# Optimization experiments

Measured on AMD Instinct MI355X. Metric: run time of the kernel, lower is better.

Reference implementation:

```python
import jax, jax.numpy as jnp
import numpy as np

N_NODES = 100000
N_EDGES = 1600000
D = 64
NUM_GROUPS = 2


def setup_inputs() -> dict:
    key = jax.random.key(0)
    k_h, k_ws, k_wg, k_src, k_dst, k_grp = jax.random.split(key, 6)
    h = jax.random.normal(k_h, (N_NODES, D), dtype=jnp.float32)
    # nn.Linear(in, out, bias=False) weights have shape [out, in]
    W_self = jax.random.normal(k_ws, (D, D), dtype=jnp.float32) * (1.0 / np.sqrt(D))
    W_groups = jax.random.normal(k_wg, (NUM_GROUPS, D, D), dtype=jnp.float32) * (1.0 / np.sqrt(D))
    src = jax.random.randint(k_src, (N_EDGES,), 0, N_NODES, dtype=jnp.int32)
    dst = jax.random.randint(k_dst, (N_EDGES,), 0, N_NODES, dtype=jnp.int32)
    group_labels = jax.random.randint(k_grp, (N_NODES,), 0, NUM_GROUPS, dtype=jnp.int32)
    return {"h": h, "W_self": W_self, "W_groups": W_groups,
            "src": src, "dst": dst, "group_labels": group_labels}


def reference(h, W_self, W_groups, src, dst, group_labels):
    # h: [N, d_in]; W_self: [d_out, d_in]; W_groups: [G, d_out, d_in]
    # Edge list (src, dst) replaces the DGL graph; message m_e = h[src_e],
    # transformed by W_groups[group[src_e]], scatter-added into dst_e.
    n_nodes = h.shape[0]
    num_groups = W_groups.shape[0]

    h_self = h @ W_self.T                       # [N, d_out]

    h_src = jnp.take(h, src, axis=0)            # [E, d_in] edge gather
    g_src = jnp.take(group_labels, src, axis=0)  # [E]

    h_agg = jnp.zeros((n_nodes, W_groups.shape[1]), dtype=h.dtype)
    for i in range(num_groups):  # small fixed loop over groups
        masked = jnp.where((g_src == i)[:, None], h_src, 0.0)  # [E, d_in]
        # Linearity lets us aggregate first, then transform (same math as
        # transforming each message then scatter_add, but far less compute).
        seg = jax.ops.segment_sum(masked, dst, num_segments=n_nodes)  # [N, d_in]
        h_agg = h_agg + seg @ W_groups[i].T      # [N, d_out]

    return h_self + h_agg
```

## Files before the change

### kernel.cpp

```cpp
#include <hip/hip_runtime.h>

#define N_NODES 100000
#define N_EDGES 1600000
#define D 64
#define NB 784
#define NR 8
#define CAPB_R 384
#define LCAP 64
#define LSTR 68
#define SRC_MASK 0x1FFFF
#define NBB 782
#define ZOFF (N_NODES * 32)

typedef unsigned int u32;
typedef short bfrag8 __attribute__((ext_vector_type(8)));
typedef float f32x4 __attribute__((ext_vector_type(4)));


__device__ inline u32 pk_bf16(float lo, float hi) {
    u32 a = __float_as_uint(lo);
    a = (a + 0x7fffu + ((a >> 16) & 1u)) >> 16;
    u32 b = __float_as_uint(hi);
    b = (b + 0x7fffu + ((b >> 16) & 1u)) & 0xffff0000u;
    return a | b;
}

__global__ __launch_bounds__(256) void prep(const float* __restrict__ h,
                                            const float* __restrict__ W_self,
                                            const float* __restrict__ W_groups,
                                            const int* __restrict__ src,
                                            const int* __restrict__ dst,
                                            const int* __restrict__ grp,
                                            int* __restrict__ bcnt,
                                            int* __restrict__ buckets,
                                            u32* __restrict__ h_bf,
                                            u32* __restrict__ Wc) {
    __shared__ int hist[NB];
    __shared__ int gbase[NB];
    const int tid = threadIdx.x;
    const int bx = blockIdx.x;

    if (bx < NBB) {
        const int r = bx & (NR - 1);
        for (int b = tid; b < NB; b += 256) hist[b] = 0;
        __syncthreads();

        int ent[8], bkt[8], rnk[8];
        const int e0 = bx * 2048;
#pragma unroll
        for (int i = 0; i < 8; ++i) {
            int e = e0 + tid + i * 256;
            if (e < N_EDGES) {
                int s = src[e], d = dst[e];
                int g = grp[s];
                bkt[i] = d >> 7;
                ent[i] = s | (g << 17) | ((d & 127) << 18);
                rnk[i] = atomicAdd(&hist[bkt[i]], 1);
            } else {
                bkt[i] = -1;
            }
        }
        __syncthreads();
        for (int b = tid; b < NB; b += 256) {
            int hc = hist[b];
            gbase[b] = hc ? atomicAdd(&bcnt[b * NR + r], hc) : 0;
        }
        __syncthreads();
#pragma unroll
        for (int i = 0; i < 8; ++i) {
            if (bkt[i] >= 0) {
                int pos = gbase[bkt[i]] + rnk[i];
                if (pos < CAPB_R)
                    buckets[(bkt[i] * NR + r) * CAPB_R + pos] = ent[i];
            }
        }
    } else if (bx < NBB + 12500) {
        int i = (bx - NBB) * 256 + tid;
        float2 v = reinterpret_cast<const float2*>(h)[i];
        h_bf[i] = pk_bf16(v.x, v.y);
    } else {
        for (int idx = tid; idx < 6144; idx += 256) {
            int j = idx / 96, kk = idx - j * 96;
            int k = kk * 2;
            float lo, hi;
            if (k < 64)       { lo = W_self[j * 64 + k];          hi = W_self[j * 64 + k + 1]; }
            else if (k < 128) { lo = W_groups[j * 64 + k - 64];   hi = W_groups[j * 64 + k - 63]; }
            else              { lo = W_groups[4096 + j * 64 + k - 128];
                                hi = W_groups[4096 + j * 64 + k - 127]; }
            Wc[j * 96 + kk] = pk_bf16(lo, hi);
        }
        if (tid < 32) h_bf[ZOFF + tid] = 0u;
    }
}

__global__ __launch_bounds__(256, 8) void gather_gemm(const u32* __restrict__ h_bf,
                                                      const int* __restrict__ bcnt,
                                                      const int* __restrict__ buckets,
                                                      const u32* __restrict__ Wc,
                                                      float* __restrict__ out) {
    __shared__ __align__(16) int lcsr[32 * LSTR];
    __shared__ int cnt0[32];
    __shared__ int cnt1[32];

    const int tid = threadIdx.x;
    const int cb = blockIdx.x >> 2;
    const int sub = blockIdx.x & 3;
    const int nbase = cb * 128 + sub * 32;
    if (nbase >= N_NODES) return;

    if (tid < 32) { cnt0[tid] = 0; cnt1[tid] = 0; }
    __syncthreads();

    {
        const int4 cA = *reinterpret_cast<const int4*>(bcnt + cb * NR);
        const int4 cB = *reinterpret_cast<const int4*>(bcnt + cb * NR + 4);
        int cns[NR] = { cA.x, cA.y, cA.z, cA.w, cB.x, cB.y, cB.z, cB.w };
#pragma unroll
        for (int r = 0; r < NR; ++r) {
            const int cnt = min(cns[r], CAPB_R);
            const int* bp = buckets + (cb * NR + r) * CAPB_R;
            for (int i = tid; i < cnt; i += 256) {
                int e = bp[i];
                if (((e >> 23) & 3) == sub) {
                    int nl = (e >> 18) & 31;
                    int off = (e & SRC_MASK) * 32;
                    if ((e >> 17) & 1) {
                        int s1 = atomicAdd(&cnt1[nl], 1);
                        if (s1 < LCAP) lcsr[nl * LSTR + (LCAP - 1 - s1)] = off;
                    } else {
                        int s0 = atomicAdd(&cnt0[nl], 1);
                        if (s0 < LCAP) lcsr[nl * LSTR + s0] = off;
                    }
                }
            }
        }
    }
    __syncthreads();

    const int wave = tid >> 6;
    const int lane = tid & 63;
    const int half = lane >> 5;
    const int c = lane & 31;

    for (int q = 0; q < 8; ++q) {
        const int nl = wave * 8 + q;
        const int base = nl * LSTR;
        const int c0 = min(cnt0[nl], LCAP);
        const int c1 = min(cnt1[nl], LCAP);
        const int imax = max(c0, c1);
        float a0l = 0.f, a0h = 0.f, a1l = 0.f, a1h = 0.f;

        for (int i = 0; i < imax; i += 8) {
            int offA[4], offB[4];
#pragma unroll
            for (int k = 0; k < 4; ++k) {
                int t = i + 2 * k + half;
                int vA = lcsr[base + t];
                int vB = lcsr[base + (LCAP - 1 - t)];
                offA[k] = (t < c0) ? vA : ZOFF;
                offB[k] = (t < c1) ? vB : ZOFF;
            }
            u32 xA[4], xB[4];
#pragma unroll
            for (int k = 0; k < 4; ++k) {
                xA[k] = h_bf[(size_t)(offA[k] + c)];
                xB[k] = h_bf[(size_t)(offB[k] + c)];
            }
#pragma unroll
            for (int k = 0; k < 4; ++k) {
                a0l += __uint_as_float(xA[k] << 16);
                a0h += __uint_as_float(xA[k] & 0xffff0000u);
                a1l += __uint_as_float(xB[k] << 16);
                a1h += __uint_as_float(xB[k] & 0xffff0000u);
            }
        }

        a0l += __shfl_xor(a0l, 32, 64);
        a0h += __shfl_xor(a0h, 32, 64);
        a1l += __shfl_xor(a1l, 32, 64);
        a1h += __shfl_xor(a1h, 32, 64);

        if (half == 0) {
            lcsr[base + c]      = (int)pk_bf16(a0l, a0h);
            lcsr[base + 32 + c] = (int)pk_bf16(a1l, a1h);
        }
    }
    __syncthreads();

    const int m = lane & 15;
    const int quad = lane >> 4;
    const int rowh = wave & 1;
    const int jth = wave >> 1;
    const int nl16 = rowh * 16 + m;
    const int arow = nbase + nl16;

    union Cvt { uint4 u; bfrag8 s; };
    bfrag8 a[6];
    const u32* ap = h_bf + (size_t)arow * 32 + quad * 4;
#pragma unroll
    for (int ks = 0; ks < 2; ++ks) {
        Cvt cv;
        cv.u = *reinterpret_cast<const uint4*>(ap + ks * 16);
        a[ks] = cv.s;
    }
#pragma unroll
    for (int ks = 2; ks < 6; ++ks) {
        Cvt cv;
        cv.u = *reinterpret_cast<const uint4*>(&lcsr[nl16 * LSTR + (ks - 2) * 16 + quad * 4]);
        a[ks] = cv.s;
    }

    f32x4 acc[2];
#pragma unroll
    for (int jj = 0; jj < 2; ++jj) acc[jj] = (f32x4){0.f, 0.f, 0.f, 0.f};

    const u32* wp = Wc + (size_t)m * 96 + quad * 4;
#pragma unroll
    for (int ks = 0; ks < 6; ++ks) {
#pragma unroll
        for (int jj = 0; jj < 2; ++jj) {
            Cvt cw;
            cw.u = *reinterpret_cast<const uint4*>(wp + (jth * 2 + jj) * 1536 + ks * 16);
            acc[jj] = __builtin_amdgcn_mfma_f32_16x16x32_bf16(a[ks], cw.s, acc[jj], 0, 0, 0);
        }
    }

    const int rbase = nbase + rowh * 16 + quad * 4;
#pragma unroll
    for (int jj = 0; jj < 2; ++jj) {
#pragma unroll
        for (int r = 0; r < 4; ++r) {
            out[(size_t)(rbase + r) * 64 + (jth * 2 + jj) * 16 + m] = acc[jj][r];
        }
    }
}

extern "C" void kernel_launch(void* const* d_in, const int* in_sizes, int n_in,
                              void* d_out, int out_size, void* d_ws, size_t ws_size,
                              hipStream_t stream) {
    const float* h        = (const float*)d_in[0];
    const float* W_self   = (const float*)d_in[1];
    const float* W_groups = (const float*)d_in[2];
    const int*   src      = (const int*)d_in[3];
    const int*   dst      = (const int*)d_in[4];
    const int*   grp      = (const int*)d_in[5];
    float*       out      = (float*)d_out;

    int* bcnt    = (int*)d_ws;
    int* buckets = bcnt + 8192;
    u32* h_bf    = (u32*)(buckets + NB * NR * CAPB_R);
    u32* Wc      = h_bf + (size_t)N_NODES * 32 + 32;

    hipMemsetAsync(bcnt, 0, NB * NR * sizeof(int), stream);

    prep<<<NBB + 12500 + 1, 256, 0, stream>>>(h, W_self, W_groups, src, dst, grp,
                                              bcnt, buckets, h_bf, Wc);
    gather_gemm<<<NB * 4, 256, 0, stream>>>(h_bf, bcnt, buckets, Wc, out);
}
```

Measured before the change: 180.8 us.

## Bucket edges per 32-node block and merge group loops into one pass

Edges are now bucketed directly by 32-node destination blocks (3125 buckets with 2 replicas) instead of 128-node buckets that four blocks each rescanned and filtered. This removes the redundant four-way bucket reads in gather_gemm. The gather loop now walks the two group lists back to back instead of padding both to the longer length, which avoids wasted zero-row loads. The costs are a larger shared histogram in prep and more contended atomics per replica. Per-replica capacity is unchanged, so overflow is unlikely.

```diff
diff --git a/kernel.cpp b/kernel.cpp
--- a/kernel.cpp
+++ b/kernel.cpp
@@ -3,8 +3,8 @@
 #define N_NODES 100000
 #define N_EDGES 1600000
 #define D 64
-#define NB 784
-#define NR 8
+#define NB2 3125
+#define NR 2
 #define CAPB_R 384
 #define LCAP 64
 #define LSTR 68
@@ -35,14 +35,14 @@
                                             int* __restrict__ buckets,
                                             u32* __restrict__ h_bf,
                                             u32* __restrict__ Wc) {
-    __shared__ int hist[NB];
-    __shared__ int gbase[NB];
+    __shared__ int hist[NB2];
+    __shared__ int gbase[NB2];
     const int tid = threadIdx.x;
     const int bx = blockIdx.x;
 
     if (bx < NBB) {
         const int r = bx & (NR - 1);
-        for (int b = tid; b < NB; b += 256) hist[b] = 0;
+        for (int b = tid; b < NB2; b += 256) hist[b] = 0;
         __syncthreads();
 
         int ent[8], bkt[8], rnk[8];
@@ -53,15 +53,15 @@
             if (e < N_EDGES) {
                 int s = src[e], d = dst[e];
                 int g = grp[s];
-                bkt[i] = d >> 7;
-                ent[i] = s | (g << 17) | ((d & 127) << 18);
+                bkt[i] = d >> 5;
+                ent[i] = s | (g << 17) | ((d & 31) << 18);
                 rnk[i] = atomicAdd(&hist[bkt[i]], 1);
             } else {
                 bkt[i] = -1;
             }
         }
         __syncthreads();
-        for (int b = tid; b < NB; b += 256) {
+        for (int b = tid; b < NB2; b += 256) {
             int hc = hist[b];
             gbase[b] = hc ? atomicAdd(&bcnt[b * NR + r], hc) : 0;
         }
@@ -99,39 +99,30 @@
                                                       const u32* __restrict__ Wc,
                                                       float* __restrict__ out) {
     __shared__ __align__(16) int lcsr[32 * LSTR];
-    __shared__ int cnt0[32];
-    __shared__ int cnt1[32];
+    __shared__ int cntg[64];
 
     const int tid = threadIdx.x;
-    const int cb = blockIdx.x >> 2;
-    const int sub = blockIdx.x & 3;
-    const int nbase = cb * 128 + sub * 32;
-    if (nbase >= N_NODES) return;
-
-    if (tid < 32) { cnt0[tid] = 0; cnt1[tid] = 0; }
+    const int cb = blockIdx.x;
+    const int nbase = cb * 32;
+
+    if (tid < 64) cntg[tid] = 0;
     __syncthreads();
 
     {
-        const int4 cA = *reinterpret_cast<const int4*>(bcnt + cb * NR);
-        const int4 cB = *reinterpret_cast<const int4*>(bcnt + cb * NR + 4);
-        int cns[NR] = { cA.x, cA.y, cA.z, cA.w, cB.x, cB.y, cB.z, cB.w };
+        const int2 cc = *reinterpret_cast<const int2*>(bcnt + cb * NR);
+        int cns[NR] = { cc.x, cc.y };
 #pragma unroll
         for (int r = 0; r < NR; ++r) {
             const int cnt = min(cns[r], CAPB_R);
             const int* bp = buckets + (cb * NR + r) * CAPB_R;
             for (int i = tid; i < cnt; i += 256) {
                 int e = bp[i];
-                if (((e >> 23) & 3) == sub) {
-                    int nl = (e >> 18) & 31;
-                    int off = (e & SRC_MASK) * 32;
-                    if ((e >> 17) & 1) {
-                        int s1 = atomicAdd(&cnt1[nl], 1);
-                        if (s1 < LCAP) lcsr[nl * LSTR + (LCAP - 1 - s1)] = off;
-                    } else {
-                        int s0 = atomicAdd(&cnt0[nl], 1);
-                        if (s0 < LCAP) lcsr[nl * LSTR + s0] = off;
-                    }
-                }
+                int nl = (e >> 18) & 31;
+                int g = (e >> 17) & 1;
+                int off = (e & SRC_MASK) * 32;
+                int idx = atomicAdd(&cntg[g * 32 + nl], 1);
+                int pos = g ? (LCAP - 1 - idx) : idx;
+                if (idx < LCAP) lcsr[nl * LSTR + pos] = off;
             }
         }
     }
@@ -145,33 +136,66 @@
     for (int q = 0; q < 8; ++q) {
         const int nl = wave * 8 + q;
         const int base = nl * LSTR;
-        const int c0 = min(cnt0[nl], LCAP);
-        const int c1 = min(cnt1[nl], LCAP);
-        const int imax = max(c0, c1);
+        const int c0 = min(cntg[nl], LCAP);
+        const int c1 = min(cntg[32 + nl], LCAP);
+        const int total = c0 + c1;
         float a0l = 0.f, a0h = 0.f, a1l = 0.f, a1h = 0.f;
 
-        for (int i = 0; i < imax; i += 8) {
-            int offA[4], offB[4];
-#pragma unroll
-            for (int k = 0; k < 4; ++k) {
-                int t = i + 2 * k + half;
-                int vA = lcsr[base + t];
-                int vB = lcsr[base + (LCAP - 1 - t)];
-                offA[k] = (t < c0) ? vA : ZOFF;
-                offB[k] = (t < c1) ? vB : ZOFF;
-            }
-            u32 xA[4], xB[4];
-#pragma unroll
-            for (int k = 0; k < 4; ++k) {
-                xA[k] = h_bf[(size_t)(offA[k] + c)];
-                xB[k] = h_bf[(size_t)(offB[k] + c)];
-            }
-#pragma unroll
-            for (int k = 0; k < 4; ++k) {
-                a0l += __uint_as_float(xA[k] << 16);
-                a0h += __uint_as_float(xA[k] & 0xffff0000u);
-                a1l += __uint_as_float(xB[k] << 16);
-                a1h += __uint_as_float(xB[k] & 0xffff0000u);
+        for (int i = 0; i < total; i += 8) {
+            if (i + 8 <= c0) {
+                int off[4];
+#pragma unroll
+                for (int k = 0; k < 4; ++k)
+                    off[k] = lcsr[base + i + 2 * k + half];
+                u32 x[4];
+#pragma unroll
+                for (int k = 0; k < 4; ++k) x[k] = h_bf[(size_t)(off[k] + c)];
+#pragma unroll
+                for (int k = 0; k < 4; ++k) {
+                    a0l += __uint_as_float(x[k] << 16);
+                    a0h += __uint_as_float(x[k] & 0xffff0000u);
+                }
+            } else if (i >= c0) {
+                int off[4];
+#pragma unroll
+                for (int k = 0; k < 4; ++k) {
+                    int u = i + 2 * k + half;
+                    int idx = (LCAP - 1 - (u - c0)) & (LCAP - 1);
+                    int v = lcsr[base + idx];
+                    off[k] = (u < total) ? v : ZOFF;
+                }
+                u32 x[4];
+#pragma unroll
+                for (int k = 0; k < 4; ++k) x[k] = h_bf[(size_t)(off[k] + c)];
+#pragma unroll
+                for (int k = 0; k < 4; ++k) {
+                    a1l += __uint_as_float(x[k] << 16);
+                    a1h += __uint_as_float(x[k] & 0xffff0000u);
+                }
+            } else {
+                int off[4];
+                bool fm[4];
+#pragma unroll
+                for (int k = 0; k < 4; ++k) {
+                    int u = i + 2 * k + half;
+                    bool f = u < c0;
+                    int idx = f ? u : ((LCAP - 1 - (u - c0)) & (LCAP - 1));
+                    int v = lcsr[base + idx];
+                    off[k] = (u < total) ? v : ZOFF;
+                    fm[k] = f;
+                }
+                u32 x[4];
+#pragma unroll
+                for (int k = 0; k < 4; ++k) x[k] = h_bf[(size_t)(off[k] + c)];
+#pragma unroll
+                for (int k = 0; k < 4; ++k) {
+                    float vl = __uint_as_float(x[k] << 16);
+                    float vh = __uint_as_float(x[k] & 0xffff0000u);
+                    a0l += fm[k] ? vl : 0.f;
+                    a0h += fm[k] ? vh : 0.f;
+                    a1l += fm[k] ? 0.f : vl;
+                    a1h += fm[k] ? 0.f : vh;
+                }
             }
         }
 
@@ -248,12 +272,12 @@
 
     int* bcnt    = (int*)d_ws;
     int* buckets = bcnt + 8192;
-    u32* h_bf    = (u32*)(buckets + NB * NR * CAPB_R);
+    u32* h_bf    = (u32*)(buckets + NB2 * NR * CAPB_R);
     u32* Wc      = h_bf + (size_t)N_NODES * 32 + 32;
 
-    hipMemsetAsync(bcnt, 0, NB * NR * sizeof(int), stream);
+    hipMemsetAsync(bcnt, 0, 8192 * sizeof(int), stream);
 
     prep<<<NBB + 12500 + 1, 256, 0, stream>>>(h, W_self, W_groups, src, dst, grp,
                                               bcnt, buckets, h_bf, Wc);
-    gather_gemm<<<NB * 4, 256, 0, stream>>>(h_bf, bcnt, buckets, Wc, out);
-}
+    gather_gemm<<<NB2, 256, 0, stream>>>(h_bf, bcnt, buckets, Wc, out);
+}
```

Result: slower. 192.3 us (+6.4%).

## Bucket edges per 32-node block and aggregate via LDS float atomics

Applied to the files above, without the earlier changes.

Edges are now binned directly into 32-node buckets with only two sub-ranks, and the two sub-counters are packed into one 32-bit word so a single atomic updates both. The gather kernel drops the per-block filter and local CSR build. Each wave instead reads bucket entries and scatter-adds bf16-expanded rows into an fp32 LDS segment buffer with shared atomics, then packs that buffer to bf16 for the MFMA stage. The h conversion uses float4 loads. This trades per-node sequential accumulation loops for many LDS atomic adds, and it raises the histogram size and the number of buckets.

```diff
diff --git a/kernel.cpp b/kernel.cpp
--- a/kernel.cpp
+++ b/kernel.cpp
@@ -3,14 +3,13 @@
 #define N_NODES 100000
 #define N_EDGES 1600000
 #define D 64
-#define NB 784
-#define NR 8
+#define NB2 3125
 #define CAPB_R 384
-#define LCAP 64
-#define LSTR 68
-#define SRC_MASK 0x1FFFF
-#define NBB 782
-#define ZOFF (N_NODES * 32)
+#define NBB 1564
+#define NTC 6250
+#define SSTR 134
+#define TSTR 68
+#define ZB ((u32)(N_NODES * 128))
 
 typedef unsigned int u32;
 typedef short bfrag8 __attribute__((ext_vector_type(8)));
@@ -31,53 +30,57 @@
                                             const int* __restrict__ src,
                                             const int* __restrict__ dst,
                                             const int* __restrict__ grp,
-                                            int* __restrict__ bcnt,
+                                            u32* __restrict__ bcnt32,
                                             int* __restrict__ buckets,
                                             u32* __restrict__ h_bf,
                                             u32* __restrict__ Wc) {
-    __shared__ int hist[NB];
-    __shared__ int gbase[NB];
+    __shared__ u32 hist[NB2];
     const int tid = threadIdx.x;
     const int bx = blockIdx.x;
 
     if (bx < NBB) {
-        const int r = bx & (NR - 1);
-        for (int b = tid; b < NB; b += 256) hist[b] = 0;
+        for (int b = tid; b < NB2; b += 256) hist[b] = 0u;
         __syncthreads();
 
-        int ent[8], bkt[8], rnk[8];
-        const int e0 = bx * 2048;
-#pragma unroll
-        for (int i = 0; i < 8; ++i) {
+        const int e0 = bx * 1024;
+        const int r = tid & 1;
+        const u32 add = r ? 0x10000u : 1u;
+        const int sh = r * 16;
+
+        u32 ent[4]; int bkt[4], rnk[4];
+#pragma unroll
+        for (int i = 0; i < 4; ++i) {
             int e = e0 + tid + i * 256;
             if (e < N_EDGES) {
                 int s = src[e], d = dst[e];
                 int g = grp[s];
-                bkt[i] = d >> 7;
-                ent[i] = s | (g << 17) | ((d & 127) << 18);
-                rnk[i] = atomicAdd(&hist[bkt[i]], 1);
+                bkt[i] = d >> 5;
+                ent[i] = ((u32)s << 7) | ((u32)g << 5) | (u32)(d & 31);
+                u32 old = atomicAdd(&hist[bkt[i]], add);
+                rnk[i] = (int)((old >> sh) & 0xffffu);
             } else {
                 bkt[i] = -1;
             }
         }
         __syncthreads();
-        for (int b = tid; b < NB; b += 256) {
-            int hc = hist[b];
-            gbase[b] = hc ? atomicAdd(&bcnt[b * NR + r], hc) : 0;
+        for (int b = tid; b < NB2; b += 256) {
+            u32 hv = hist[b];
+            if (hv) hist[b] = atomicAdd(&bcnt32[b], hv);
         }
         __syncthreads();
 #pragma unroll
-        for (int i = 0; i < 8; ++i) {
+        for (int i = 0; i < 4; ++i) {
             if (bkt[i] >= 0) {
-                int pos = gbase[bkt[i]] + rnk[i];
+                int pos = (int)((hist[bkt[i]] >> sh) & 0xffffu) + rnk[i];
                 if (pos < CAPB_R)
-                    buckets[(bkt[i] * NR + r) * CAPB_R + pos] = ent[i];
+                    buckets[(bkt[i] * 2 + r) * CAPB_R + pos] = (int)ent[i];
             }
         }
-    } else if (bx < NBB + 12500) {
+    } else if (bx < NBB + NTC) {
         int i = (bx - NBB) * 256 + tid;
-        float2 v = reinterpret_cast<const float2*>(h)[i];
-        h_bf[i] = pk_bf16(v.x, v.y);
+        float4 v = reinterpret_cast<const float4*>(h)[i];
+        h_bf[2 * i]     = pk_bf16(v.x, v.y);
+        h_bf[2 * i + 1] = pk_bf16(v.z, v.w);
     } else {
         for (int idx = tid; idx < 6144; idx += 256) {
             int j = idx / 96, kk = idx - j * 96;
@@ -89,101 +92,85 @@
                                 hi = W_groups[4096 + j * 64 + k - 127]; }
             Wc[j * 96 + kk] = pk_bf16(lo, hi);
         }
-        if (tid < 32) h_bf[ZOFF + tid] = 0u;
+        if (tid < 32) h_bf[N_NODES * 32 + tid] = 0u;
     }
 }
 
 __global__ __launch_bounds__(256, 8) void gather_gemm(const u32* __restrict__ h_bf,
-                                                      const int* __restrict__ bcnt,
+                                                      const u32* __restrict__ bcnt32,
                                                       const int* __restrict__ buckets,
                                                       const u32* __restrict__ Wc,
                                                       float* __restrict__ out) {
-    __shared__ __align__(16) int lcsr[32 * LSTR];
-    __shared__ int cnt0[32];
-    __shared__ int cnt1[32];
-
+    __shared__ __align__(16) float seg[17 * 256];
     const int tid = threadIdx.x;
-    const int cb = blockIdx.x >> 2;
-    const int sub = blockIdx.x & 3;
-    const int nbase = cb * 128 + sub * 32;
-    if (nbase >= N_NODES) return;
-
-    if (tid < 32) { cnt0[tid] = 0; cnt1[tid] = 0; }
-    __syncthreads();
-
-    {
-        const int4 cA = *reinterpret_cast<const int4*>(bcnt + cb * NR);
-        const int4 cB = *reinterpret_cast<const int4*>(bcnt + cb * NR + 4);
-        int cns[NR] = { cA.x, cA.y, cA.z, cA.w, cB.x, cB.y, cB.z, cB.w };
-#pragma unroll
-        for (int r = 0; r < NR; ++r) {
-            const int cnt = min(cns[r], CAPB_R);
-            const int* bp = buckets + (cb * NR + r) * CAPB_R;
-            for (int i = tid; i < cnt; i += 256) {
-                int e = bp[i];
-                if (((e >> 23) & 3) == sub) {
-                    int nl = (e >> 18) & 31;
-                    int off = (e & SRC_MASK) * 32;
-                    if ((e >> 17) & 1) {
-                        int s1 = atomicAdd(&cnt1[nl], 1);
-                        if (s1 < LCAP) lcsr[nl * LSTR + (LCAP - 1 - s1)] = off;
-                    } else {
-                        int s0 = atomicAdd(&cnt0[nl], 1);
-                        if (s0 < LCAP) lcsr[nl * LSTR + s0] = off;
-                    }
-                }
-            }
-        }
-    }
+    const int cb = blockIdx.x;
+    const int nbase = cb * 32;
+
+#pragma unroll
+    for (int k = 0; k < 17; ++k) seg[tid + k * 256] = 0.f;
     __syncthreads();
 
     const int wave = tid >> 6;
     const int lane = tid & 63;
-    const int half = lane >> 5;
-    const int c = lane & 31;
-
-    for (int q = 0; q < 8; ++q) {
-        const int nl = wave * 8 + q;
-        const int base = nl * LSTR;
-        const int c0 = min(cnt0[nl], LCAP);
-        const int c1 = min(cnt1[nl], LCAP);
-        const int imax = max(c0, c1);
-        float a0l = 0.f, a0h = 0.f, a1l = 0.f, a1h = 0.f;
-
-        for (int i = 0; i < imax; i += 8) {
-            int offA[4], offB[4];
-#pragma unroll
-            for (int k = 0; k < 4; ++k) {
-                int t = i + 2 * k + half;
-                int vA = lcsr[base + t];
-                int vB = lcsr[base + (LCAP - 1 - t)];
-                offA[k] = (t < c0) ? vA : ZOFF;
-                offB[k] = (t < c1) ? vB : ZOFF;
-            }
-            u32 xA[4], xB[4];
-#pragma unroll
-            for (int k = 0; k < 4; ++k) {
-                xA[k] = h_bf[(size_t)(offA[k] + c)];
-                xB[k] = h_bf[(size_t)(offB[k] + c)];
-            }
-#pragma unroll
-            for (int k = 0; k < 4; ++k) {
-                a0l += __uint_as_float(xA[k] << 16);
-                a0h += __uint_as_float(xA[k] & 0xffff0000u);
-                a1l += __uint_as_float(xB[k] << 16);
-                a1h += __uint_as_float(xB[k] & 0xffff0000u);
-            }
-        }
-
-        a0l += __shfl_xor(a0l, 32, 64);
-        a0h += __shfl_xor(a0h, 32, 64);
-        a1l += __shfl_xor(a1l, 32, 64);
-        a1h += __shfl_xor(a1h, 32, 64);
-
-        if (half == 0) {
-            lcsr[base + c]      = (int)pk_bf16(a0l, a0h);
-            lcsr[base + 32 + c] = (int)pk_bf16(a1l, a1h);
-        }
+    const int qd = lane >> 4;
+    const int sl = lane & 15;
+    const char* hb = (const char*)h_bf;
+
+    const u32 cv = bcnt32[cb];
+    const int cnt[2] = { min((int)(cv & 0xffffu), CAPB_R),
+                         min((int)(cv >> 16), CAPB_R) };
+
+#pragma unroll
+    for (int r = 0; r < 2; ++r) {
+        const int cn = cnt[r];
+        const int* bp = buckets + (cb * 2 + r) * CAPB_R;
+        int i = wave * 4;
+        for (; i + 4 <= cn; i += 16) {
+            u32 ent = (u32)bp[i + qd];
+            u32 off = ent & 0xFFFFFF80u;
+            int nl = (int)(ent & 31u);
+            int g  = (int)((ent >> 5) & 1u);
+            uint2 p = *reinterpret_cast<const uint2*>(hb + (off + (u32)(sl * 8)));
+            float* sp = &seg[nl * SSTR + g * 64 + sl * 4];
+            atomicAdd(sp + 0, __uint_as_float(p.x << 16));
+            atomicAdd(sp + 1, __uint_as_float(p.x & 0xffff0000u));
+            atomicAdd(sp + 2, __uint_as_float(p.y << 16));
+            atomicAdd(sp + 3, __uint_as_float(p.y & 0xffff0000u));
+        }
+        if (i < cn) {
+            int idx = i + qd;
+            int sidx = idx < cn ? idx : 0;
+            u32 ent = (u32)bp[sidx];
+            if (idx >= cn) ent = ZB;
+            u32 off = ent & 0xFFFFFF80u;
+            int nl = (int)(ent & 31u);
+            int g  = (int)((ent >> 5) & 1u);
+            uint2 p = *reinterpret_cast<const uint2*>(hb + (off + (u32)(sl * 8)));
+            float* sp = &seg[nl * SSTR + g * 64 + sl * 4];
+            atomicAdd(sp + 0, __uint_as_float(p.x << 16));
+            atomicAdd(sp + 1, __uint_as_float(p.x & 0xffff0000u));
+            atomicAdd(sp + 2, __uint_as_float(p.y << 16));
+            atomicAdd(sp + 3, __uint_as_float(p.y & 0xffff0000u));
+        }
+    }
+    __syncthreads();
+
+    u32 pk[8];
+#pragma unroll
+    for (int k = 0; k < 8; ++k) {
+        int idx = tid + k * 256;
+        int nl = idx >> 6, col = idx & 63;
+        int g = col >> 5, cp = col & 31;
+        const float* sp = &seg[nl * SSTR + g * 64 + cp * 2];
+        pk[k] = pk_bf16(sp[0], sp[1]);
+    }
+    __syncthreads();
+    u32* tile = reinterpret_cast<u32*>(seg);
+#pragma unroll
+    for (int k = 0; k < 8; ++k) {
+        int idx = tid + k * 256;
+        int nl = idx >> 6, col = idx & 63;
+        tile[nl * TSTR + col] = pk[k];
     }
     __syncthreads();
 
@@ -199,15 +186,15 @@
     const u32* ap = h_bf + (size_t)arow * 32 + quad * 4;
 #pragma unroll
     for (int ks = 0; ks < 2; ++ks) {
-        Cvt cv;
-        cv.u = *reinterpret_cast<const uint4*>(ap + ks * 16);
-        a[ks] = cv.s;
+        Cvt cv2;
+        cv2.u = *reinterpret_cast<const uint4*>(ap + ks * 16);
+        a[ks] = cv2.s;
     }
 #pragma unroll
     for (int ks = 2; ks < 6; ++ks) {
-        Cvt cv;
-        cv.u = *reinterpret_cast<const uint4*>(&lcsr[nl16 * LSTR + (ks - 2) * 16 + quad * 4]);
-        a[ks] = cv.s;
+        Cvt cv2;
+        cv2.u = *reinterpret_cast<const uint4*>(&tile[nl16 * TSTR + (ks - 2) * 16 + quad * 4]);
+        a[ks] = cv2.s;
     }
 
     f32x4 acc[2];
@@ -229,8 +216,8 @@
 #pragma unroll
     for (int jj = 0; jj < 2; ++jj) {
 #pragma unroll
-        for (int r = 0; r < 4; ++r) {
-            out[(size_t)(rbase + r) * 64 + (jth * 2 + jj) * 16 + m] = acc[jj][r];
+        for (int r2 = 0; r2 < 4; ++r2) {
+            out[(size_t)(rbase + r2) * 64 + (jth * 2 + jj) * 16 + m] = acc[jj][r2];
         }
     }
 }
@@ -246,14 +233,14 @@
     const int*   grp      = (const int*)d_in[5];
     float*       out      = (float*)d_out;
 
-    int* bcnt    = (int*)d_ws;
-    int* buckets = bcnt + 8192;
-    u32* h_bf    = (u32*)(buckets + NB * NR * CAPB_R);
+    u32* bcnt32  = (u32*)d_ws;
+    int* buckets = (int*)(bcnt32 + 8192);
+    u32* h_bf    = (u32*)(buckets + NB2 * 2 * CAPB_R);
     u32* Wc      = h_bf + (size_t)N_NODES * 32 + 32;
 
-    hipMemsetAsync(bcnt, 0, NB * NR * sizeof(int), stream);
-
-    prep<<<NBB + 12500 + 1, 256, 0, stream>>>(h, W_self, W_groups, src, dst, grp,
-                                              bcnt, buckets, h_bf, Wc);
-    gather_gemm<<<NB * 4, 256, 0, stream>>>(h_bf, bcnt, buckets, Wc, out);
-}
+    hipMemsetAsync(bcnt32, 0, NB2 * sizeof(u32), stream);
+
+    prep<<<NBB + NTC + 1, 256, 0, stream>>>(h, W_self, W_groups, src, dst, grp,
+                                            bcnt32, buckets, h_bf, Wc);
+    gather_gemm<<<NB2, 256, 0, stream>>>(h_bf, bcnt32, buckets, Wc, out);
+}
```

Measured after the change: 717.6 us. 3.97x slower.
